# Kernel tuning notes

Measured on AMD Instinct MI355X. Metric: run time of the kernel, lower is better.

## Reference

```python
import jax, jax.numpy as jnp
import numpy as np

D = 512
N_LAYERS = 2


def _ran_scan(x_seq, c0, Wx_c, Wc_c, b_c, reverse):
    """RAN cell scanned over time. x_seq: [L,B,D]; c0: [B,D].
    Wx_c: [D,3D] (i, f, ctilde from x); Wc_c: [D,2D] (i, f from carry); b_c: [3D].
    Residual: h = tanh(c) + x. Returns (hs [L,B,D] in original time order, c_final)."""
    gx_seq = jnp.einsum('lbd,de->lbe', x_seq, Wx_c) + b_c  # precompute input projections

    def step(c, inp):
        x, gx = inp
        gi, gf, gc = gx[:, :D], gx[:, D:2 * D], gx[:, 2 * D:]
        gcarry = c @ Wc_c  # [B,2D]
        i = jax.nn.sigmoid(gi + gcarry[:, :D])
        f = jax.nn.sigmoid(gf + gcarry[:, D:])
        c_new = i * gc + f * c
        h = jnp.tanh(c_new) + x
        return c_new, h

    c_fin, hs = jax.lax.scan(step, c0, (x_seq, gx_seq), reverse=reverse)
    return hs, c_fin


def setup_inputs() -> dict:
    key = jax.random.key(0)
    k1, k2, k3, k4 = jax.random.split(key, 4)
    L, B, V = 512, 64, 32004
    scale = 1.0 / np.sqrt(D)
    xs = jax.random.randint(k1, (L, B), 0, 32000, dtype=jnp.int64)
    emb = jax.random.normal(k2, (V, D), dtype=jnp.float32) * 0.1
    Wx = jax.random.normal(k3, (4, D, 3 * D), dtype=jnp.float32) * scale
    Wc = jax.random.normal(k4, (4, D, 2 * D), dtype=jnp.float32) * scale
    b = jnp.zeros((4, 3 * D), dtype=jnp.float32)
    return {"xs": xs, "emb": emb, "Wx": Wx, "Wc": Wc, "b": b}


def reference(xs, emb, Wx, Wc, b):
    L, B = xs.shape
    x_es = emb[xs]  # [L,B,D] embedding lookup
    c = jnp.zeros((B, D), dtype=emb.dtype)  # c0
    for layer in range(N_LAYERS):
        fw = layer * 2
        bw = layer * 2 + 1
        # snaker: forward-direction RAN, carry c threads into backward pass
        first, c = _ran_scan(x_es, c, Wx[fw], Wc[fw], b[fw], reverse=False)
        x_es, c = _ran_scan(first, c, Wx[bw], Wc[bw], b[bw], reverse=True)
    return x_es
```

## Files before the change

kernel.cpp:

```cpp
#include <hip/hip_runtime.h>
#include <hip/hip_bf16.h>

#define DD 512
#define LL 512
#define BB 64
#define NT 1536
#define MROWS (LL*BB)

typedef short short8 __attribute__((ext_vector_type(8)));
typedef float floatx4 __attribute__((ext_vector_type(4)));
union U4S8 { uint4 u4; short8 s8; };
typedef unsigned long long ull;

static __device__ __forceinline__ unsigned short f2bf(float f) {
  unsigned int u = __float_as_uint(f);
  unsigned int r = (u + 0x7fffu + ((u >> 16) & 1u)) >> 16;
  return (unsigned short)r;
}
static __device__ __forceinline__ float bf2f(unsigned short s) {
  return __uint_as_float(((unsigned int)s) << 16);
}

__global__ void pack_wc_k(const float* __restrict__ Wc, unsigned int* __restrict__ Wp) {
  int U = blockIdx.x * 256 + threadIdx.x;
  int sdg = U >> 15;
  int s = sdg >> 3, dg = sdg & 7;
  int r = U & 32767;
  int u = r & 3;
  int lane = (r >> 2) & 63;
  int fidx = r >> 8;
  int kt = fidx & 1;
  int ct = (fidx >> 1) & 7;
  int w = fidx >> 4;
  int k = w * 64 + kt * 32 + 8 * (lane >> 4) + 2 * u;
  int cl = ct * 16 + (lane & 15);
  int gcol = (cl >> 6) * 512 + dg * 64 + (cl & 63);
  size_t base = (size_t)s * DD * 1024;
  float lo = Wc[base + (size_t)k * 1024 + gcol];
  float hi = Wc[base + (size_t)(k + 1) * 1024 + gcol];
  Wp[U] = (unsigned int)f2bf(lo) | ((unsigned int)f2bf(hi) << 16);
}

__global__ __launch_bounds__(256)
void pack_wx_k(const float* __restrict__ W, unsigned short* __restrict__ Wxp) {
  __shared__ float t[64][65];
  int k0 = blockIdx.x * 64, n0 = blockIdx.y * 64, s = blockIdx.z;
  int tx = threadIdx.x & 63, ty = threadIdx.x >> 6;
  const float* Wb = W + (size_t)s * DD * NT;
#pragma unroll
  for (int i = 0; i < 16; ++i) {
    int k = ty * 16 + i;
    t[k][tx] = Wb[(size_t)(k0 + k) * NT + n0 + tx];
  }
  __syncthreads();
  unsigned short* Ob = Wxp + (size_t)s * NT * DD;
#pragma unroll
  for (int i = 0; i < 16; ++i) {
    int n = ty * 16 + i;
    Ob[(size_t)(n0 + n) * DD + k0 + tx] = f2bf(t[tx][n]);
  }
}

__global__ void gather_k(const int* __restrict__ xs, const float* __restrict__ emb,
                         float* __restrict__ x) {
  int i = blockIdx.x * 256 + threadIdx.x;
  int row = i >> 7;
  int col = i & 127;
  const float4* src = (const float4*)(emb + (size_t)xs[row] * DD);
  ((float4*)(x + (size_t)row * DD))[col] = src[col];
}

__global__ __launch_bounds__(256)
void gemm_k(const float* __restrict__ A, const float* __restrict__ W,
            const float* __restrict__ bias, unsigned short* __restrict__ C) {
  __shared__ float As[16][128];
  __shared__ float Bs[16][128];
  const int tid = threadIdx.x;
  const int tx = tid & 15;
  const int ty = tid >> 4;
  const int m0 = blockIdx.y * 128;
  const int n0 = blockIdx.x * 128;
  const int lm = tid >> 1;
  const int lk = (tid & 1) * 8;
  const int wk = tid >> 4;
  const int wn = (tid & 15) * 8;
  float acc[8][8];
#pragma unroll
  for (int i = 0; i < 8; ++i)
#pragma unroll
    for (int j = 0; j < 8; ++j) acc[i][j] = 0.f;
  for (int k0 = 0; k0 < DD; k0 += 16) {
    float4 a0 = *(const float4*)(A + (size_t)(m0 + lm) * DD + k0 + lk);
    float4 a1 = *(const float4*)(A + (size_t)(m0 + lm) * DD + k0 + lk + 4);
    float4 w0 = *(const float4*)(W + (size_t)(k0 + wk) * NT + n0 + wn);
    float4 w1 = *(const float4*)(W + (size_t)(k0 + wk) * NT + n0 + wn + 4);
    __syncthreads();
    As[lk + 0][lm] = a0.x; As[lk + 1][lm] = a0.y; As[lk + 2][lm] = a0.z; As[lk + 3][lm] = a0.w;
    As[lk + 4][lm] = a1.x; As[lk + 5][lm] = a1.y; As[lk + 6][lm] = a1.z; As[lk + 7][lm] = a1.w;
    *(float4*)&Bs[wk][wn] = w0;
    *(float4*)&Bs[wk][wn + 4] = w1;
    __syncthreads();
#pragma unroll
    for (int kk = 0; kk < 16; ++kk) {
      float a[8], w[8];
      *(float4*)&a[0] = *(const float4*)&As[kk][ty * 8];
      *(float4*)&a[4] = *(const float4*)&As[kk][ty * 8 + 4];
      *(float4*)&w[0] = *(const float4*)&Bs[kk][tx * 8];
      *(float4*)&w[4] = *(const float4*)&Bs[kk][tx * 8 + 4];
#pragma unroll
      for (int i = 0; i < 8; ++i)
#pragma unroll
        for (int j = 0; j < 8; ++j)
          acc[i][j] = fmaf(a[i], w[j], acc[i][j]);
    }
  }
#pragma unroll
  for (int i = 0; i < 8; ++i) {
    size_t rb = (size_t)(m0 + ty * 8 + i) * NT + n0 + tx * 8;
#pragma unroll
    for (int jv = 0; jv < 2; ++jv) {
      ushort4 v;
      v.x = f2bf(acc[i][jv*4+0] + bias[n0 + tx*8 + jv*4 + 0]);
      v.y = f2bf(acc[i][jv*4+1] + bias[n0 + tx*8 + jv*4 + 1]);
      v.z = f2bf(acc[i][jv*4+2] + bias[n0 + tx*8 + jv*4 + 2]);
      v.w = f2bf(acc[i][jv*4+3] + bias[n0 + tx*8 + jv*4 + 3]);
      *(ushort4*)(C + rb + jv*4) = v;
    }
  }
}

__global__ __launch_bounds__(256)
void gemm_m_k(const float* __restrict__ A, const unsigned short* __restrict__ Wt,
              const float* __restrict__ bias, unsigned short* __restrict__ C) {
  __shared__ unsigned short Al[128 * 40];
  __shared__ unsigned short Bl[128 * 40];
  const int tid = threadIdx.x;
  const int m0 = blockIdx.y * 128, n0 = blockIdx.x * 128;
  const int wave = tid >> 6, lane = tid & 63;
  const int wm = wave >> 1, wn = wave & 1;
  const int l15 = lane & 15, lh = lane >> 4;
  floatx4 acc[4][4];
#pragma unroll
  for (int i = 0; i < 4; ++i)
#pragma unroll
    for (int j = 0; j < 4; ++j) acc[i][j] = (floatx4){0.f, 0.f, 0.f, 0.f};

  const int ar = tid >> 3, ac = (tid & 7) * 4;
  const int br = tid >> 2, bc = (tid & 3) * 8;
#pragma unroll 1
  for (int k0 = 0; k0 < DD; k0 += 32) {
    float4 av[4];
#pragma unroll
    for (int p = 0; p < 4; ++p)
      av[p] = *(const float4*)(A + (size_t)(m0 + ar + p * 32) * DD + k0 + ac);
    uint4 bv0 = *(const uint4*)(Wt + (size_t)(n0 + br) * DD + k0 + bc);
    uint4 bv1 = *(const uint4*)(Wt + (size_t)(n0 + br + 64) * DD + k0 + bc);
    __syncthreads();
#pragma unroll
    for (int p = 0; p < 4; ++p) {
      ushort4 w4;
      w4.x = f2bf(av[p].x); w4.y = f2bf(av[p].y);
      w4.z = f2bf(av[p].z); w4.w = f2bf(av[p].w);
      *(ushort4*)&Al[(ar + p * 32) * 40 + ac] = w4;
    }
    *(uint4*)&Bl[br * 40 + bc] = bv0;
    *(uint4*)&Bl[(br + 64) * 40 + bc] = bv1;
    __syncthreads();
    U4S8 af[4], bf[4];
#pragma unroll
    for (int mf = 0; mf < 4; ++mf)
      af[mf].u4 = *(const uint4*)&Al[(wm * 64 + mf * 16 + l15) * 40 + lh * 8];
#pragma unroll
    for (int nf = 0; nf < 4; ++nf)
      bf[nf].u4 = *(const uint4*)&Bl[(wn * 64 + nf * 16 + l15) * 40 + lh * 8];
#pragma unroll
    for (int mf = 0; mf < 4; ++mf)
#pragma unroll
      for (int nf = 0; nf < 4; ++nf)
        acc[mf][nf] = __builtin_amdgcn_mfma_f32_16x16x32_bf16(
            af[mf].s8, bf[nf].s8, acc[mf][nf], 0, 0, 0);
  }
#pragma unroll
  for (int nf = 0; nf < 4; ++nf) {
    int n = n0 + wn * 64 + nf * 16 + l15;
    float bn = bias[n];
#pragma unroll
    for (int mf = 0; mf < 4; ++mf) {
      int row = m0 + wm * 64 + mf * 16 + lh * 4;
      size_t base = (size_t)row * NT + n;
#pragma unroll
      for (int e = 0; e < 4; ++e)
        C[base + (size_t)e * NT] = f2bf(acc[mf][nf][e] + bn);
    }
  }
}

__global__ __launch_bounds__(512, 1)
void scan_k(const unsigned short* __restrict__ gx,
            const uint4* __restrict__ Wsc,
            const float* __restrict__ xin,
            float* __restrict__ hout,
            float* __restrict__ cbuf,
            unsigned short* __restrict__ xbu,
            unsigned int* __restrict__ flags,
            int reverse, unsigned int step_base) {
  __shared__ float pd[8192];
  const int tid = threadIdx.x;
  const int bg = blockIdx.x & 7;
  const int dg = blockIdx.x >> 3;
  const int lane = tid & 63;
  const int w = tid >> 6;
  const int batch = bg * 8 + w;
  const int dim = dg * 64 + lane;

  uint4 Wf[16];
  {
    const uint4* ws = Wsc + (size_t)dg * 8192;
#pragma unroll
    for (int f = 0; f < 16; ++f)
      Wf[f] = ws[(size_t)(w * 16 + f) * 64 + lane];
  }
  float c_reg = cbuf[batch * DD + dim];
  int t0 = reverse ? (LL - 1) : 0;
  size_t r0 = (size_t)t0 * BB + batch;
  float g_i = bf2f(gx[r0 * NT + dim]);
  float g_f = bf2f(gx[r0 * NT + 512 + dim]);
  float g_c = bf2f(gx[r0 * NT + 1024 + dim]);
  float x_v = xin[r0 * DD + dim];
  const int arow = lane & 7, lh = lane >> 4;

#pragma unroll 1
  for (int s = 0; s < LL; ++s) {
    unsigned int need = step_base + (unsigned int)s;
    {
      const unsigned int* f = flags + bg * 8 + w;
      while (__hip_atomic_load(f, __ATOMIC_RELAXED, __HIP_MEMORY_SCOPE_AGENT) < need)
        __builtin_amdgcn_s_sleep(1);
    }
    const ull* src = (const ull*)xbu + (size_t)(((s + 1) & 1)) * 8192;
    int ai = (bg * 8 + arow) * 128 + w * 16 + 2 * lh;
    ull v0 = __hip_atomic_load(&src[ai],     __ATOMIC_RELAXED, __HIP_MEMORY_SCOPE_AGENT);
    ull v1 = __hip_atomic_load(&src[ai + 1], __ATOMIC_RELAXED, __HIP_MEMORY_SCOPE_AGENT);
    ull v2 = __hip_atomic_load(&src[ai + 8], __ATOMIC_RELAXED, __HIP_MEMORY_SCOPE_AGENT);
    ull v3 = __hip_atomic_load(&src[ai + 9], __ATOMIC_RELAXED, __HIP_MEMORY_SCOPE_AGENT);
    int sn = (s + 1 < LL) ? s + 1 : s;
    int tn = reverse ? (LL - 1 - sn) : sn;
    size_t rn = (size_t)tn * BB + batch;
    float ngi = bf2f(gx[rn * NT + dim]);
    float ngf = bf2f(gx[rn * NT + 512 + dim]);
    float ngc = bf2f(gx[rn * NT + 1024 + dim]);
    float nxv = xin[rn * DD + dim];
    U4S8 A0, A1;
    A0.u4 = make_uint4((unsigned int)v0, (unsigned int)(v0 >> 32),
                       (unsigned int)v1, (unsigned int)(v1 >> 32));
    A1.u4 = make_uint4((unsigned int)v2, (unsigned int)(v2 >> 32),
                       (unsigned int)v3, (unsigned int)(v3 >> 32));
#pragma unroll
    for (int ct = 0; ct < 8; ++ct) {
      U4S8 B0, B1; B0.u4 = Wf[ct * 2]; B1.u4 = Wf[ct * 2 + 1];
      floatx4 acc = __builtin_amdgcn_mfma_f32_16x16x32_bf16(
          A0.s8, B0.s8, (floatx4){0.f, 0.f, 0.f, 0.f}, 0, 0, 0);
      acc = __builtin_amdgcn_mfma_f32_16x16x32_bf16(A1.s8, B1.s8, acc, 0, 0, 0);
      if (lane < 32) {
        int colb = ct * 16 + (lane & 15);
        int rb = (lane >> 4) * 4;
#pragma unroll
        for (int e = 0; e < 4; ++e)
          pd[(w * 8 + rb + e) * 128 + colb] = acc[e];
      }
    }
    __syncthreads();
    float gsi = 0.f, gsf = 0.f;
#pragma unroll
    for (int ww = 0; ww < 8; ++ww) {
      gsi += pd[(ww * 8 + w) * 128 + lane];
      gsf += pd[(ww * 8 + w) * 128 + 64 + lane];
    }
    float iv = 1.f / (1.f + __expf(-(g_i + gsi)));
    float fv = 1.f / (1.f + __expf(-(g_f + gsf)));
    float cn = fmaf(fv, c_reg, iv * g_c);
    c_reg = cn;
    __hip_atomic_store(xbu + (size_t)((s & 1)) * 32768 + batch * DD + dim,
                       f2bf(cn), __ATOMIC_RELAXED, __HIP_MEMORY_SCOPE_AGENT);
    int t = reverse ? (LL - 1 - s) : s;
    size_t rowg = (size_t)t * BB + batch;
    hout[rowg * DD + dim] = tanhf(cn) + x_v;
    g_i = ngi; g_f = ngf; g_c = ngc; x_v = nxv;
    __syncthreads();
    if (tid == 0)
      __hip_atomic_store(&flags[bg * 8 + dg], need + 1u,
                         __ATOMIC_RELAXED, __HIP_MEMORY_SCOPE_AGENT);
  }
  cbuf[batch * DD + dim] = c_reg;
}

extern "C" void kernel_launch(void* const* d_in, const int* in_sizes, int n_in,
                              void* d_out, int out_size, void* d_ws, size_t ws_size,
                              hipStream_t stream) {
  const int* xs = (const int*)d_in[0];
  const float* emb = (const float*)d_in[1];
  const float* Wx = (const float*)d_in[2];
  const float* Wc = (const float*)d_in[3];
  const float* bias = (const float*)d_in[4];
  float* out = (float*)d_out;
  char* ws = (char*)d_ws;

  unsigned short* gx = (unsigned short*)ws;
  float* xB = (float*)(ws + (size_t)100663296);
  unsigned int* Wp = (unsigned int*)(ws + (size_t)167772160);
  float* cbuf = (float*)(ws + (size_t)171966464);
  unsigned short* xbu = (unsigned short*)(ws + (size_t)172097536);
  unsigned int* flags = (unsigned int*)(ws + (size_t)172228608);
  unsigned short* Wxp = (unsigned short*)(ws + (size_t)172229632);
  const size_t NEED = 178521088ull;
  const bool use_mfma_gemm = (ws_size >= NEED);

  hipMemsetAsync(cbuf, 0, 131072, stream);
  hipMemsetAsync(xbu, 0, 131072, stream);
  hipMemsetAsync(flags, 0, 256, stream);
  pack_wc_k<<<4096, 256, 0, stream>>>(Wc, Wp);
  if (use_mfma_gemm)
    pack_wx_k<<<dim3(8, 24, 4), 256, 0, stream>>>(Wx, Wxp);
  gather_k<<<MROWS * 128 / 256, 256, 0, stream>>>(xs, emb, out);

  for (int s = 0; s < 4; ++s) {
    const float* xin = (s % 2 == 0) ? out : xB;
    float* xout = (s % 2 == 0) ? xB : out;
    if (use_mfma_gemm)
      gemm_m_k<<<dim3(NT / 128, MROWS / 128), 256, 0, stream>>>(
          xin, Wxp + (size_t)s * NT * DD, bias + (size_t)s * NT, gx);
    else
      gemm_k<<<dim3(NT / 128, MROWS / 128), 256, 0, stream>>>(
          xin, Wx + (size_t)s * DD * NT, bias + (size_t)s * NT, gx);
    scan_k<<<64, 512, 0, stream>>>(
        gx, (const uint4*)(Wp + (size_t)s * 262144), xin, xout, cbuf, xbu, flags,
        s & 1, (unsigned int)(s * 512));
  }
}
```

Baseline: 5.847 ms.

## Replace per-block flag barrier with step-tagged data words in scan exchange

The recurrent scan previously published each step's bf16 carry, then did a block barrier and set a per-block flag that consumers polled before reading the data. Now each 32-bit word carries the bf16 value in the high half and a 16-bit step tag in the low half. Consumers spin directly on the data until all tags match, which removes the second __syncthreads and the separate flag round-trip. The LDS partial-sum buffer is double-buffered so the dropped barrier does not create a write-after-read hazard. The cost is twice the exchange traffic and a dependence on tag wraparound staying correct.

```diff
diff --git a/kernel.cpp b/kernel.cpp
--- a/kernel.cpp
+++ b/kernel.cpp
@@ -166,19 +166,19 @@
     *(uint4*)&Bl[br * 40 + bc] = bv0;
     *(uint4*)&Bl[(br + 64) * 40 + bc] = bv1;
     __syncthreads();
-    U4S8 af[4], bf[4];
+    U4S8 af[4], bfr[4];
 #pragma unroll
     for (int mf = 0; mf < 4; ++mf)
       af[mf].u4 = *(const uint4*)&Al[(wm * 64 + mf * 16 + l15) * 40 + lh * 8];
 #pragma unroll
     for (int nf = 0; nf < 4; ++nf)
-      bf[nf].u4 = *(const uint4*)&Bl[(wn * 64 + nf * 16 + l15) * 40 + lh * 8];
+      bfr[nf].u4 = *(const uint4*)&Bl[(wn * 64 + nf * 16 + l15) * 40 + lh * 8];
 #pragma unroll
     for (int mf = 0; mf < 4; ++mf)
 #pragma unroll
       for (int nf = 0; nf < 4; ++nf)
         acc[mf][nf] = __builtin_amdgcn_mfma_f32_16x16x32_bf16(
-            af[mf].s8, bf[nf].s8, acc[mf][nf], 0, 0, 0);
+            af[mf].s8, bfr[nf].s8, acc[mf][nf], 0, 0, 0);
   }
 #pragma unroll
   for (int nf = 0; nf < 4; ++nf) {
@@ -201,10 +201,9 @@
             const float* __restrict__ xin,
             float* __restrict__ hout,
             float* __restrict__ cbuf,
-            unsigned short* __restrict__ xbu,
-            unsigned int* __restrict__ flags,
+            unsigned int* __restrict__ xbt,
             int reverse, unsigned int step_base) {
-  __shared__ float pd[8192];
+  __shared__ float pd[2][8192];
   const int tid = threadIdx.x;
   const int bg = blockIdx.x & 7;
   const int dg = blockIdx.x >> 3;
@@ -228,21 +227,30 @@
   float g_c = bf2f(gx[r0 * NT + 1024 + dim]);
   float x_v = xin[r0 * DD + dim];
   const int arow = lane & 7, lh = lane >> 4;
+  const int ai0 = (bg * 8 + arow) * 256 + w * 32 + lh * 4;
 
 #pragma unroll 1
   for (int s = 0; s < LL; ++s) {
-    unsigned int need = step_base + (unsigned int)s;
+    unsigned int wtag = (step_base + (unsigned int)s) & 0xffffu;
+    const ull* sp = (const ull*)xbt + (size_t)((s + 1) & 1) * 16384 + ai0;
+    ull q0, q1, q2, q3, q4, q5, q6, q7;
     {
-      const unsigned int* f = flags + bg * 8 + w;
-      while (__hip_atomic_load(f, __ATOMIC_RELAXED, __HIP_MEMORY_SCOPE_AGENT) < need)
+      ull tp = (ull)wtag * 0x0000000100000001ull;
+      for (;;) {
+        q0 = __hip_atomic_load(sp + 0,  __ATOMIC_RELAXED, __HIP_MEMORY_SCOPE_AGENT);
+        q1 = __hip_atomic_load(sp + 1,  __ATOMIC_RELAXED, __HIP_MEMORY_SCOPE_AGENT);
+        q2 = __hip_atomic_load(sp + 2,  __ATOMIC_RELAXED, __HIP_MEMORY_SCOPE_AGENT);
+        q3 = __hip_atomic_load(sp + 3,  __ATOMIC_RELAXED, __HIP_MEMORY_SCOPE_AGENT);
+        q4 = __hip_atomic_load(sp + 16, __ATOMIC_RELAXED, __HIP_MEMORY_SCOPE_AGENT);
+        q5 = __hip_atomic_load(sp + 17, __ATOMIC_RELAXED, __HIP_MEMORY_SCOPE_AGENT);
+        q6 = __hip_atomic_load(sp + 18, __ATOMIC_RELAXED, __HIP_MEMORY_SCOPE_AGENT);
+        q7 = __hip_atomic_load(sp + 19, __ATOMIC_RELAXED, __HIP_MEMORY_SCOPE_AGENT);
+        ull d = ((q0 ^ tp) | (q1 ^ tp) | (q2 ^ tp) | (q3 ^ tp) |
+                 (q4 ^ tp) | (q5 ^ tp) | (q6 ^ tp) | (q7 ^ tp)) & 0x0000ffff0000ffffull;
+        if (__all(d == 0)) break;
         __builtin_amdgcn_s_sleep(1);
-    }
-    const ull* src = (const ull*)xbu + (size_t)(((s + 1) & 1)) * 8192;
-    int ai = (bg * 8 + arow) * 128 + w * 16 + 2 * lh;
-    ull v0 = __hip_atomic_load(&src[ai],     __ATOMIC_RELAXED, __HIP_MEMORY_SCOPE_AGENT);
-    ull v1 = __hip_atomic_load(&src[ai + 1], __ATOMIC_RELAXED, __HIP_MEMORY_SCOPE_AGENT);
-    ull v2 = __hip_atomic_load(&src[ai + 8], __ATOMIC_RELAXED, __HIP_MEMORY_SCOPE_AGENT);
-    ull v3 = __hip_atomic_load(&src[ai + 9], __ATOMIC_RELAXED, __HIP_MEMORY_SCOPE_AGENT);
+      }
+    }
     int sn = (s + 1 < LL) ? s + 1 : s;
     int tn = reverse ? (LL - 1 - sn) : sn;
     size_t rn = (size_t)tn * BB + batch;
@@ -251,10 +259,17 @@
     float ngc = bf2f(gx[rn * NT + 1024 + dim]);
     float nxv = xin[rn * DD + dim];
     U4S8 A0, A1;
-    A0.u4 = make_uint4((unsigned int)v0, (unsigned int)(v0 >> 32),
-                       (unsigned int)v1, (unsigned int)(v1 >> 32));
-    A1.u4 = make_uint4((unsigned int)v2, (unsigned int)(v2 >> 32),
-                       (unsigned int)v3, (unsigned int)(v3 >> 32));
+    A0.u4 = make_uint4(
+        ((unsigned int)q0 >> 16) | ((unsigned int)(q0 >> 32) & 0xffff0000u),
+        ((unsigned int)q1 >> 16) | ((unsigned int)(q1 >> 32) & 0xffff0000u),
+        ((unsigned int)q2 >> 16) | ((unsigned int)(q2 >> 32) & 0xffff0000u),
+        ((unsigned int)q3 >> 16) | ((unsigned int)(q3 >> 32) & 0xffff0000u));
+    A1.u4 = make_uint4(
+        ((unsigned int)q4 >> 16) | ((unsigned int)(q4 >> 32) & 0xffff0000u),
+        ((unsigned int)q5 >> 16) | ((unsigned int)(q5 >> 32) & 0xffff0000u),
+        ((unsigned int)q6 >> 16) | ((unsigned int)(q6 >> 32) & 0xffff0000u),
+        ((unsigned int)q7 >> 16) | ((unsigned int)(q7 >> 32) & 0xffff0000u));
+    float* pds = pd[s & 1];
 #pragma unroll
     for (int ct = 0; ct < 8; ++ct) {
       U4S8 B0, B1; B0.u4 = Wf[ct * 2]; B1.u4 = Wf[ct * 2 + 1];
@@ -266,30 +281,28 @@
         int rb = (lane >> 4) * 4;
 #pragma unroll
         for (int e = 0; e < 4; ++e)
-          pd[(w * 8 + rb + e) * 128 + colb] = acc[e];
+          pds[(w * 8 + rb + e) * 128 + colb] = acc[e];
       }
     }
     __syncthreads();
     float gsi = 0.f, gsf = 0.f;
 #pragma unroll
     for (int ww = 0; ww < 8; ++ww) {
-      gsi += pd[(ww * 8 + w) * 128 + lane];
-      gsf += pd[(ww * 8 + w) * 128 + 64 + lane];
+      gsi += pds[(ww * 8 + w) * 128 + lane];
+      gsf += pds[(ww * 8 + w) * 128 + 64 + lane];
     }
     float iv = 1.f / (1.f + __expf(-(g_i + gsi)));
     float fv = 1.f / (1.f + __expf(-(g_f + gsf)));
     float cn = fmaf(fv, c_reg, iv * g_c);
     c_reg = cn;
-    __hip_atomic_store(xbu + (size_t)((s & 1)) * 32768 + batch * DD + dim,
-                       f2bf(cn), __ATOMIC_RELAXED, __HIP_MEMORY_SCOPE_AGENT);
+    unsigned int outw = ((unsigned int)f2bf(cn) << 16)
+                        | ((step_base + (unsigned int)s + 1u) & 0xffffu);
+    __hip_atomic_store(xbt + (size_t)(s & 1) * 32768 + batch * DD + dim, outw,
+                       __ATOMIC_RELAXED, __HIP_MEMORY_SCOPE_AGENT);
     int t = reverse ? (LL - 1 - s) : s;
     size_t rowg = (size_t)t * BB + batch;
     hout[rowg * DD + dim] = tanhf(cn) + x_v;
     g_i = ngi; g_f = ngf; g_c = ngc; x_v = nxv;
-    __syncthreads();
-    if (tid == 0)
-      __hip_atomic_store(&flags[bg * 8 + dg], need + 1u,
-                         __ATOMIC_RELAXED, __HIP_MEMORY_SCOPE_AGENT);
   }
   cbuf[batch * DD + dim] = c_reg;
 }
@@ -309,15 +322,13 @@
   float* xB = (float*)(ws + (size_t)100663296);
   unsigned int* Wp = (unsigned int*)(ws + (size_t)167772160);
   float* cbuf = (float*)(ws + (size_t)171966464);
-  unsigned short* xbu = (unsigned short*)(ws + (size_t)172097536);
-  unsigned int* flags = (unsigned int*)(ws + (size_t)172228608);
-  unsigned short* Wxp = (unsigned short*)(ws + (size_t)172229632);
-  const size_t NEED = 178521088ull;
+  unsigned int* xbt = (unsigned int*)(ws + (size_t)172097536);
+  unsigned short* Wxp = (unsigned short*)(ws + (size_t)172359680);
+  const size_t NEED = 178651136ull;
   const bool use_mfma_gemm = (ws_size >= NEED);
 
   hipMemsetAsync(cbuf, 0, 131072, stream);
-  hipMemsetAsync(xbu, 0, 131072, stream);
-  hipMemsetAsync(flags, 0, 256, stream);
+  hipMemsetAsync(xbt, 0, 262144, stream);
   pack_wc_k<<<4096, 256, 0, stream>>>(Wc, Wp);
   if (use_mfma_gemm)
     pack_wx_k<<<dim3(8, 24, 4), 256, 0, stream>>>(Wx, Wxp);
@@ -333,7 +344,7 @@
       gemm_k<<<dim3(NT / 128, MROWS / 128), 256, 0, stream>>>(
           xin, Wx + (size_t)s * DD * NT, bias + (size_t)s * NT, gx);
     scan_k<<<64, 512, 0, stream>>>(
-        gx, (const uint4*)(Wp + (size_t)s * 262144), xin, xout, cbuf, xbu, flags,
+        gx, (const uint4*)(Wp + (size_t)s * 262144), xin, xout, cbuf, xbt,
         s & 1, (unsigned int)(s * 512));
   }
 }
```

Measured after the change: 8.083 ms. +38.2%, slower.
